# Kernel optimization log

Hardware: AMD Instinct MI355X
Metric: run time of the kernel (lower is better)

Reference implementation:

```python
import jax, jax.numpy as jnp
import numpy as np

B, C_IN, C_OUT, RANK, MODES, N = 32, 64, 64, 16, 64, 8192


def setup_inputs() -> dict:
    key = jax.random.key(0)
    k0, k1, k2, k3, k4 = jax.random.split(key, 5)
    x = jax.random.normal(k0, (B, C_IN, N), dtype=jnp.float32)
    U_r = jax.random.normal(k1, (C_IN, RANK), dtype=jnp.float32)
    U_i = jax.random.normal(k2, (C_IN, RANK), dtype=jnp.float32)
    V_r = jax.random.normal(k3, (RANK, C_OUT), dtype=jnp.float32)
    V_i = jax.random.normal(k4, (RANK, C_OUT), dtype=jnp.float32)
    S = jnp.ones((RANK,), dtype=jnp.float32)
    return {"x": x, "U_r": U_r, "U_i": U_i, "V_r": V_r, "V_i": V_i, "S": S}


def reference(x, U_r, U_i, V_r, V_i, S):
    # rFFT over spatial dim, orthonormal normalization (matches torch norm='ortho')
    x_fft = jnp.fft.rfft(x, axis=-1, norm='ortho')          # [B, C_in, N//2+1] complex
    n_freq = x_fft.shape[-1]
    modes = min(MODES, n_freq)
    x_modes = x_fft[..., :modes]                             # [B, C_in, modes]

    U = U_r + 1j * U_i                                       # [C_in, rank]
    V = V_r + 1j * V_i                                       # [rank, C_out]
    # w = (U * S) @ V, then slice first `modes` output channels (as in source)
    w = jnp.einsum('ir,ro->io', U * S[None, :].astype(U.dtype), V)
    w = w[..., :modes]                                       # no-op when C_out == modes

    out_modes = jnp.einsum('bix,io->box', x_modes, w)        # [B, C_out, modes]
    # zero-fill remaining spectrum (equivalent to zeros_like + slice assign)
    full = jnp.pad(out_modes, ((0, 0), (0, 0), (0, n_freq - modes)))
    return jnp.fft.irfft(full, n=x.shape[-1], axis=-1, norm='ortho')
```

## Files before the change

kernel.cpp:

```cpp
#include <hip/hip_runtime.h>

#define NPTS   8192
#define BATCH  32
#define CIN    64
#define COUT   64
#define RANKK  16
#define ROWS   (BATCH * CIN)
#define KB_SPLIT 16

typedef _Float16 f16;
typedef _Float16 f16x2 __attribute__((ext_vector_type(2)));
typedef _Float16 f16x8 __attribute__((ext_vector_type(8)));
typedef float    f32x2 __attribute__((ext_vector_type(2)));
typedef float    f32x4 __attribute__((ext_vector_type(4)));

__device__ __forceinline__ void gload16(const void* g, void* l) {
  __builtin_amdgcn_global_load_lds(
      (const __attribute__((address_space(1))) void*)g,
      (__attribute__((address_space(3))) void*)l, 16, 0, 0);
}

__global__ __launch_bounds__(256) void build_tables(f16* __restrict__ T,
                                                    f16* __restrict__ Tt) {
  __shared__ f16 tile[128][18];
  const int n0 = blockIdx.x * 16;
  const int t = threadIdx.x;
#pragma unroll
  for (int j = 0; j < 8; ++j) {
    int flat = t + 256 * j;
    int c = flat >> 4, dn = flat & 15;
    int k = c & 63, n = n0 + dn;
    int m = (k * n) & (NPTS - 1);
    float ang = (float)m * (6.28318530717958647692f / (float)NPTS);
    float sv, cv;
    sincosf(ang, &sv, &cv);
    tile[c][dn] = (f16)((c < 64) ? cv : sv);
  }
  __syncthreads();
#pragma unroll
  for (int j = 0; j < 8; ++j) {
    int flat = t + 256 * j;
    int c = flat >> 4, dn = flat & 15;
    T[(size_t)c * NPTS + n0 + dn] = tile[c][dn];
  }
#pragma unroll
  for (int j = 0; j < 8; ++j) {
    int flat = t + 256 * j;
    int dn = flat >> 7, c = flat & 127;
    Tt[(size_t)(n0 + dn) * 128 + c] = tile[c][dn];
  }
}

__global__ __launch_bounds__(256) void fwd_dft(const float* __restrict__ x,
                                               const f16* __restrict__ T,
                                               f16* __restrict__ Sp) {
  __shared__ __align__(16) char lds[3 * 16384];
  const int t    = threadIdx.x;
  const int w    = t >> 6;
  const int lane = t & 63;
  const int rl = lane & 15, hi = lane >> 4;
  const int kb = blockIdx.x & (KB_SPLIT - 1);
  const int r0 = (blockIdx.x >> 4) * 64;
  const int k0 = kb * (NPTS / KB_SPLIT);

  const int xc0 = t, xc1 = t + 256;
  const int tc0 = t, tc1 = t + 256;
  const int xr0_ = xc0 >> 3, xr1_ = xc1 >> 3;
  const int tr0_ = tc0 >> 2, tr1_ = tc1 >> 2;
  const int xo0 = ((xc0 & 7) ^ (xr0_ & 7)) << 2;
  const int xo1 = ((xc1 & 7) ^ (xr1_ & 7)) << 2;
  const int to0 = ((tc0 & 3) ^ (tr0_ & 3)) << 3;
  const int to1 = ((tc1 & 3) ^ (tr1_ & 3)) << 3;
  const float* xs0 = x + (size_t)(r0 + xr0_) * NPTS + k0 + xo0;
  const float* xs1 = x + (size_t)(r0 + xr1_) * NPTS + k0 + xo1;
  const f16*   ts0 = T + (size_t)tr0_ * NPTS + k0 + to0;
  const f16*   ts1 = T + (size_t)tr1_ * NPTS + k0 + to1;
  const int wu = w * 64 * 16;

  auto STAGE = [&](int kt, int slot) {
    char* xb = lds + slot * 16384;
    char* tb = xb + 8192;
    const int kk = kt * 32;
    gload16(xs0 + kk, xb + wu);
    gload16(xs1 + kk, xb + 4096 + wu);
    gload16(ts0 + kk, tb + wu);
    gload16(ts1 + kk, tb + 4096 + wu);
  };

  f32x4 acc[8];
#pragma unroll
  for (int i = 0; i < 8; ++i) acc[i] = (f32x4){0.f, 0.f, 0.f, 0.f};

  const int axr = w * 16 + rl;
  const int ad0 = (axr * 8 + ((2 * hi) ^ (axr & 7))) * 16;
  const int ad1 = (axr * 8 + ((2 * hi + 1) ^ (axr & 7))) * 16;
  int bd[8];
#pragma unroll
  for (int ct = 0; ct < 8; ++ct) {
    int trow = ct * 16 + rl;
    bd[ct] = (trow * 4 + (hi ^ (trow & 3))) * 16;
  }

  auto COMPUTE = [&](int slot) {
    char* xb = lds + slot * 16384;
    char* tb = xb + 8192;
    f32x4 a0 = *(const f32x4*)(xb + ad0);
    f32x4 a1 = *(const f32x4*)(xb + ad1);
    f16x8 af;
#pragma unroll
    for (int j = 0; j < 4; ++j) { af[j] = (f16)a0[j]; af[4 + j] = (f16)a1[j]; }
#pragma unroll
    for (int ct = 0; ct < 8; ++ct) {
      f16x8 bf = *(const f16x8*)(tb + bd[ct]);
      acc[ct] = __builtin_amdgcn_mfma_f32_16x16x32_f16(af, bf, acc[ct], 0, 0, 0);
    }
  };

  STAGE(0, 0);
  STAGE(1, 1);
  asm volatile("s_waitcnt vmcnt(4)" ::: "memory");
  __builtin_amdgcn_s_barrier();

  int sc = 0, ss = 2;
  for (int kt = 0; kt < 16; ++kt) {
    if (kt + 2 < 16) STAGE(kt + 2, ss);
    COMPUTE(sc);
    if (kt < 15) {
      if (kt + 2 < 16)
        asm volatile("s_waitcnt vmcnt(4)" ::: "memory");
      else
        asm volatile("s_waitcnt vmcnt(0)" ::: "memory");
      __builtin_amdgcn_s_barrier();
    }
    sc = (sc == 2) ? 0 : sc + 1;
    ss = (ss == 2) ? 0 : ss + 1;
  }

  f16* out = Sp + ((size_t)kb * ROWS + r0 + w * 16) * 128;
#pragma unroll
  for (int ct = 0; ct < 8; ++ct)
#pragma unroll
    for (int i = 0; i < 4; ++i)
      out[(hi * 4 + i) * 128 + ct * 16 + rl] = (f16)acc[ct][i];
}

__global__ __launch_bounds__(256) void mix_fused(const f16* __restrict__ Sp,
                                                 const float* __restrict__ Ur,
                                                 const float* __restrict__ Ui,
                                                 const float* __restrict__ Vr,
                                                 const float* __restrict__ Vi,
                                                 const float* __restrict__ Sv,
                                                 f16* __restrict__ Qh) {
  __shared__ float Srs[64][64], Sis[64][64];
  __shared__ float wr_s[64][4], wi_s[64][4];
  const int b  = blockIdx.x >> 4;
  const int og = blockIdx.x & 15;
  const int t  = threadIdx.x;

  float accs[4][8];
#pragma unroll
  for (int j = 0; j < 4; ++j)
#pragma unroll
    for (int e = 0; e < 8; ++e) accs[j][e] = 0.f;
  for (int seg = 0; seg < KB_SPLIT; ++seg) {
    const f16* base = Sp + (size_t)seg * (ROWS * 128) + (size_t)b * 64 * 128;
#pragma unroll
    for (int j = 0; j < 4; ++j) {
      f16x8 v = *(const f16x8*)(base + (j * 256 + t) * 8);
#pragma unroll
      for (int e = 0; e < 8; ++e) accs[j][e] += (float)v[e];
    }
  }
#pragma unroll
  for (int j = 0; j < 4; ++j) {
    int d = j * 256 + t, i = d >> 4, cc = (d & 15) * 8;
    float* dst = (cc < 64) ? &Srs[i][cc] : &Sis[i][cc - 64];
#pragma unroll
    for (int e = 0; e < 8; ++e) dst[e] = accs[j][e];
  }

  {
    int i = t >> 2, ol = t & 3, o = og * 4 + ol;
    float wr = 0.f, wi = 0.f;
#pragma unroll
    for (int r = 0; r < RANKK; ++r) {
      float ur = Ur[i * RANKK + r], ui = Ui[i * RANKK + r];
      float vr = Vr[r * COUT + o],  vi = Vi[r * COUT + o];
      float s = Sv[r];
      wr += s * (ur * vr - ui * vi);
      wi += s * (ur * vi + ui * vr);
    }
    wr_s[i][ol] = wr;
    wi_s[i][ol] = wi;
  }
  __syncthreads();

  const int ol = t >> 6, k = t & 63, o = og * 4 + ol;
  float qr = 0.f, qi = 0.f;
#pragma unroll 4
  for (int i = 0; i < 64; ++i) {
    float sr = Srs[i][k], si = Sis[i][k];
    float wr = wr_s[i][ol], wi = wi_s[i][ol];
    qr += sr * wr + si * wi;
    qi += sr * wi - si * wr;
  }
  float sk = (k == 0 ? 1.0f : 2.0f) / (float)NPTS;
  f16* qrow = Qh + ((size_t)(b * 64 + o)) * 128;
  qrow[k]      = (f16)(qr * sk);
  qrow[64 + k] = (f16)(-qi * sk);
}

__global__ __launch_bounds__(256) void inv_dft(const f16* __restrict__ Qh,
                                               const f16* __restrict__ Tt,
                                               float* __restrict__ y) {
  __shared__ f16   Bt[64][136];
  __shared__ float Tr[4][16][68];
  const int t = threadIdx.x, w = t >> 6, lane = t & 63;
  const int rl = lane & 15, hi = lane >> 4;
  const int nb = blockIdx.x & 127;
  const int rb = blockIdx.x >> 7;
  const int n0 = nb * 64, r0 = rb * 64;

  f16x8 stg[4];
#pragma unroll
  for (int j = 0; j < 4; ++j) {
    int d = j * 256 + t, row = d >> 4, q = d & 15;
    stg[j] = *(const f16x8*)(Tt + (size_t)(n0 + row) * 128 + q * 8);
  }
  const f16* qrow = Qh + (size_t)(r0 + w * 16 + rl) * 128 + 8 * hi;
  f16x8 af[4];
#pragma unroll
  for (int ksv = 0; ksv < 4; ++ksv) af[ksv] = *(const f16x8*)(qrow + ksv * 32);
#pragma unroll
  for (int j = 0; j < 4; ++j) {
    int d = j * 256 + t, row = d >> 4, q = d & 15;
    *(f16x8*)(&Bt[row][q * 8]) = stg[j];
  }
  __syncthreads();

  f32x4 acc[4];
#pragma unroll
  for (int i = 0; i < 4; ++i) acc[i] = (f32x4){0.f, 0.f, 0.f, 0.f};

#pragma unroll
  for (int ksv = 0; ksv < 4; ++ksv)
#pragma unroll
    for (int s = 0; s < 4; ++s) {
      f16x8 bf = *(const f16x8*)(&Bt[s * 16 + rl][(ksv * 4 + hi) * 8]);
      acc[s] = __builtin_amdgcn_mfma_f32_16x16x32_f16(af[ksv], bf, acc[s], 0, 0, 0);
    }

#pragma unroll
  for (int s = 0; s < 4; ++s)
#pragma unroll
    for (int i = 0; i < 4; ++i)
      Tr[w][hi * 4 + i][s * 16 + rl] = acc[s][i];
#pragma unroll
  for (int p = 0; p < 4; ++p) {
    int r = p * 4 + hi;
    f32x4 v = *(const f32x4*)(&Tr[w][r][rl * 4]);
    *(f32x4*)(y + (size_t)(r0 + w * 16 + r) * NPTS + n0 + rl * 4) = v;
  }
}

extern "C" void kernel_launch(void* const* d_in, const int* in_sizes, int n_in,
                              void* d_out, int out_size, void* d_ws, size_t ws_size,
                              hipStream_t stream) {
  const float* x  = (const float*)d_in[0];
  const float* Ur = (const float*)d_in[1];
  const float* Ui = (const float*)d_in[2];
  const float* Vr = (const float*)d_in[3];
  const float* Vi = (const float*)d_in[4];
  const float* Sv = (const float*)d_in[5];
  float* y = (float*)d_out;
  char* ws = (char*)d_ws;

  f16*   T    = (f16*)ws;
  f16*   Tt   = (f16*)(ws + (2u << 20));
  f16*   Sp   = (f16*)(ws + (4u << 20));
  f16*   Qh   = (f16*)(ws + (4u << 20) +
                       (size_t)KB_SPLIT * ROWS * 128 * 2);

  build_tables<<<NPTS / 16, 256, 0, stream>>>(T, Tt);
  fwd_dft<<<(ROWS / 64) * KB_SPLIT, 256, 0, stream>>>(x, T, Sp);
  mix_fused<<<BATCH * 16, 256, 0, stream>>>(Sp, Ur, Ui, Vr, Vi, Sv, Qh);
  inv_dft<<<(ROWS / 64) * (NPTS / 64), 256, 0, stream>>>(Qh, Tt, y);
}
```

Baseline: 57.20 us.

## Halve twiddle-table build via half-period symmetry, deepen fwd pipeline, factor mix through rank

The twiddle table builder now computes only the first half of the sample points. It writes the second half using the (-1)^k symmetry of cos/sin at n+N/2, which halves the sincos work and the grid. The forward DFT pipeline grows from 3 to 4 LDS stages, so it issues one more tile of loads ahead at the cost of more shared memory. The channel-mixing kernel no longer builds the full 64x64 complex weight per block. It projects the spectrum through the rank-16 U and then V, using one 1024-thread block per batch and reducing each Sp segment once instead of 16 times.

Measured after the change: 56.44 us. No clear change (-1.3%).

```diff
diff --git a/kernel.cpp b/kernel.cpp
--- a/kernel.cpp
+++ b/kernel.cpp
@@ -9,9 +9,7 @@
 #define KB_SPLIT 16
 
 typedef _Float16 f16;
-typedef _Float16 f16x2 __attribute__((ext_vector_type(2)));
 typedef _Float16 f16x8 __attribute__((ext_vector_type(8)));
-typedef float    f32x2 __attribute__((ext_vector_type(2)));
 typedef float    f32x4 __attribute__((ext_vector_type(4)));
 
 __device__ __forceinline__ void gload16(const void* g, void* l) {
@@ -41,20 +39,26 @@
   for (int j = 0; j < 8; ++j) {
     int flat = t + 256 * j;
     int c = flat >> 4, dn = flat & 15;
-    T[(size_t)c * NPTS + n0 + dn] = tile[c][dn];
+    f16 v = tile[c][dn];
+    f16 vm = ((c & 1) ? (f16)(-v) : v);
+    T[(size_t)c * NPTS + n0 + dn] = v;
+    T[(size_t)c * NPTS + n0 + dn + NPTS / 2] = vm;
   }
 #pragma unroll
   for (int j = 0; j < 8; ++j) {
     int flat = t + 256 * j;
     int dn = flat >> 7, c = flat & 127;
-    Tt[(size_t)(n0 + dn) * 128 + c] = tile[c][dn];
+    f16 v = tile[c][dn];
+    f16 vm = ((c & 1) ? (f16)(-v) : v);
+    Tt[(size_t)(n0 + dn) * 128 + c] = v;
+    Tt[(size_t)(n0 + dn + NPTS / 2) * 128 + c] = vm;
   }
 }
 
 __global__ __launch_bounds__(256) void fwd_dft(const float* __restrict__ x,
                                                const f16* __restrict__ T,
                                                f16* __restrict__ Sp) {
-  __shared__ __align__(16) char lds[3 * 16384];
+  __shared__ __align__(16) char lds[4 * 16384];
   const int t    = threadIdx.x;
   const int w    = t >> 6;
   const int lane = t & 63;
@@ -118,22 +122,22 @@
 
   STAGE(0, 0);
   STAGE(1, 1);
-  asm volatile("s_waitcnt vmcnt(4)" ::: "memory");
+  STAGE(2, 2);
+  asm volatile("s_waitcnt vmcnt(8)" ::: "memory");
   __builtin_amdgcn_s_barrier();
 
-  int sc = 0, ss = 2;
   for (int kt = 0; kt < 16; ++kt) {
-    if (kt + 2 < 16) STAGE(kt + 2, ss);
-    COMPUTE(sc);
+    if (kt + 3 < 16) STAGE(kt + 3, (kt + 3) & 3);
+    COMPUTE(kt & 3);
     if (kt < 15) {
-      if (kt + 2 < 16)
+      if (kt <= 12)
+        asm volatile("s_waitcnt vmcnt(8)" ::: "memory");
+      else if (kt == 13)
         asm volatile("s_waitcnt vmcnt(4)" ::: "memory");
       else
         asm volatile("s_waitcnt vmcnt(0)" ::: "memory");
       __builtin_amdgcn_s_barrier();
     }
-    sc = (sc == 2) ? 0 : sc + 1;
-    ss = (ss == 2) ? 0 : ss + 1;
   }
 
   f16* out = Sp + ((size_t)kb * ROWS + r0 + w * 16) * 128;
@@ -144,7 +148,7 @@
       out[(hi * 4 + i) * 128 + ct * 16 + rl] = (f16)acc[ct][i];
 }
 
-__global__ __launch_bounds__(256) void mix_fused(const f16* __restrict__ Sp,
+__global__ __launch_bounds__(1024) void mix_rank(const f16* __restrict__ Sp,
                                                  const float* __restrict__ Ur,
                                                  const float* __restrict__ Ui,
                                                  const float* __restrict__ Vr,
@@ -152,62 +156,62 @@
                                                  const float* __restrict__ Sv,
                                                  f16* __restrict__ Qh) {
   __shared__ float Srs[64][64], Sis[64][64];
-  __shared__ float wr_s[64][4], wi_s[64][4];
-  const int b  = blockIdx.x >> 4;
-  const int og = blockIdx.x & 15;
-  const int t  = threadIdx.x;
-
-  float accs[4][8];
-#pragma unroll
-  for (int j = 0; j < 4; ++j)
-#pragma unroll
-    for (int e = 0; e < 8; ++e) accs[j][e] = 0.f;
-  for (int seg = 0; seg < KB_SPLIT; ++seg) {
-    const f16* base = Sp + (size_t)seg * (ROWS * 128) + (size_t)b * 64 * 128;
+  __shared__ float Pr[64][16], Pi[64][16];
+  const int b = blockIdx.x;
+  const int t = threadIdx.x;
+
+  {
+    float accs[8];
+#pragma unroll
+    for (int e = 0; e < 8; ++e) accs[e] = 0.f;
+    const f16* base = Sp + (size_t)b * 64 * 128 + (size_t)t * 8;
+    for (int seg = 0; seg < KB_SPLIT; ++seg) {
+      f16x8 v = *(const f16x8*)(base + (size_t)seg * (ROWS * 128));
+#pragma unroll
+      for (int e = 0; e < 8; ++e) accs[e] += (float)v[e];
+    }
+    int i = t >> 4, cc = (t & 15) * 8;
+    float* dst = (cc < 64) ? &Srs[i][cc] : &Sis[i][cc - 64];
+#pragma unroll
+    for (int e = 0; e < 8; ++e) dst[e] = accs[e];
+  }
+  __syncthreads();
+
+  {
+    const int k = t >> 4, r = t & 15;
+    float pr = 0.f, pi = 0.f;
+#pragma unroll 8
+    for (int i = 0; i < 64; ++i) {
+      float sr = Srs[i][k], si = Sis[i][k];
+      float ur = Ur[i * RANKK + r], ui = Ui[i * RANKK + r];
+      pr += sr * ur + si * ui;
+      pi += sr * ui - si * ur;
+    }
+    float s = Sv[r];
+    Pr[k][r] = pr * s;
+    Pi[k][r] = pi * s;
+  }
+  __syncthreads();
+
+  {
+    const int o = t & 63, kq = t >> 6;
+    f16* qrow = Qh + ((size_t)(b * 64 + o)) * 128;
 #pragma unroll
     for (int j = 0; j < 4; ++j) {
-      f16x8 v = *(const f16x8*)(base + (j * 256 + t) * 8);
-#pragma unroll
-      for (int e = 0; e < 8; ++e) accs[j][e] += (float)v[e];
-    }
-  }
-#pragma unroll
-  for (int j = 0; j < 4; ++j) {
-    int d = j * 256 + t, i = d >> 4, cc = (d & 15) * 8;
-    float* dst = (cc < 64) ? &Srs[i][cc] : &Sis[i][cc - 64];
-#pragma unroll
-    for (int e = 0; e < 8; ++e) dst[e] = accs[j][e];
-  }
-
-  {
-    int i = t >> 2, ol = t & 3, o = og * 4 + ol;
-    float wr = 0.f, wi = 0.f;
-#pragma unroll
-    for (int r = 0; r < RANKK; ++r) {
-      float ur = Ur[i * RANKK + r], ui = Ui[i * RANKK + r];
-      float vr = Vr[r * COUT + o],  vi = Vi[r * COUT + o];
-      float s = Sv[r];
-      wr += s * (ur * vr - ui * vi);
-      wi += s * (ur * vi + ui * vr);
-    }
-    wr_s[i][ol] = wr;
-    wi_s[i][ol] = wi;
-  }
-  __syncthreads();
-
-  const int ol = t >> 6, k = t & 63, o = og * 4 + ol;
-  float qr = 0.f, qi = 0.f;
-#pragma unroll 4
-  for (int i = 0; i < 64; ++i) {
-    float sr = Srs[i][k], si = Sis[i][k];
-    float wr = wr_s[i][ol], wi = wi_s[i][ol];
-    qr += sr * wr + si * wi;
-    qi += sr * wi - si * wr;
-  }
-  float sk = (k == 0 ? 1.0f : 2.0f) / (float)NPTS;
-  f16* qrow = Qh + ((size_t)(b * 64 + o)) * 128;
-  qrow[k]      = (f16)(qr * sk);
-  qrow[64 + k] = (f16)(-qi * sk);
+      int k = kq * 4 + j;
+      float qr = 0.f, qi = 0.f;
+#pragma unroll
+      for (int r = 0; r < RANKK; ++r) {
+        float pr = Pr[k][r], pi = Pi[k][r];
+        float vr = Vr[r * COUT + o], vi = Vi[r * COUT + o];
+        qr += pr * vr - pi * vi;
+        qi += pr * vi + pi * vr;
+      }
+      float sk = (k == 0 ? 1.0f : 2.0f) / (float)NPTS;
+      qrow[k]      = (f16)(qr * sk);
+      qrow[64 + k] = (f16)(-qi * sk);
+    }
+  }
 }
 
 __global__ __launch_bounds__(256) void inv_dft(const f16* __restrict__ Qh,
@@ -281,8 +285,8 @@
   f16*   Qh   = (f16*)(ws + (4u << 20) +
                        (size_t)KB_SPLIT * ROWS * 128 * 2);
 
-  build_tables<<<NPTS / 16, 256, 0, stream>>>(T, Tt);
+  build_tables<<<NPTS / 32, 256, 0, stream>>>(T, Tt);
   fwd_dft<<<(ROWS / 64) * KB_SPLIT, 256, 0, stream>>>(x, T, Sp);
-  mix_fused<<<BATCH * 16, 256, 0, stream>>>(Sp, Ur, Ui, Vr, Vi, Sv, Qh);
+  mix_rank<<<BATCH, 1024, 0, stream>>>(Sp, Ur, Ui, Vr, Vi, Sv, Qh);
   inv_dft<<<(ROWS / 64) * (NPTS / 64), 256, 0, stream>>>(Qh, Tt, y);
 }
```
